# Kernel tuning notes

Hardware: AMD Instinct MI355X
Metric: run time of the kernel (lower is better)

Reference implementation:

```python
import jax, jax.numpy as jnp
import numpy as np

WH, WW = 8, 8          # window_size
NUM_HEADS = 16
DIM = 512
NW = 64                # windows per image (mask leading dim)
BATCH = 16             # images
N = WH * WW            # tokens per window


def _relative_position_index():
    coords = np.stack(np.meshgrid(np.arange(WH), np.arange(WW), indexing='ij'))  # (2,Wh,Ww)
    cf = coords.reshape(2, -1)                                                   # (2,N)
    rel = cf[:, :, None] - cf[:, None, :]                                        # (2,N,N)
    rel = rel.transpose(1, 2, 0).astype(np.int64)                                # (N,N,2)
    rel[:, :, 0] += WH - 1
    rel[:, :, 1] += WW - 1
    rel[:, :, 0] *= 2 * WW - 1
    return jnp.asarray(rel.sum(-1), dtype=jnp.int32)                             # (N,N)


def setup_inputs() -> dict:
    key = jax.random.key(0)
    ks = jax.random.split(key, 8)
    B_ = BATCH * NW
    x = jax.random.normal(ks[0], (B_, N, DIM), dtype=jnp.float32)
    # 0 / -100 additive shift-style mask (Swin uses -100.0 for masked pairs)
    mraw = jax.random.uniform(ks[1], (NW, N, N))
    mask = jnp.where(mraw < 0.15, jnp.float32(-100.0), jnp.float32(0.0))
    qkv_w = jax.random.normal(ks[2], (3 * DIM, DIM), dtype=jnp.float32) * (DIM ** -0.5)
    qkv_b = jnp.zeros((3 * DIM,), dtype=jnp.float32)
    proj_w = jax.random.normal(ks[3], (DIM, DIM), dtype=jnp.float32) * (DIM ** -0.5)
    proj_b = jnp.zeros((DIM,), dtype=jnp.float32)
    n_rel = (2 * WH - 1) * (2 * WW - 1)  # 225
    rpb_table = jax.random.normal(ks[4], (n_rel, NUM_HEADS), dtype=jnp.float32) * 0.02
    rel_index = _relative_position_index()
    return {"x": x, "mask": mask, "qkv_w": qkv_w, "qkv_b": qkv_b,
            "proj_w": proj_w, "proj_b": proj_b, "rpb_table": rpb_table,
            "rel_index": rel_index}


def reference(x, mask, qkv_w, qkv_b, proj_w, proj_b, rpb_table, rel_index):
    B_, n, C = x.shape
    H = NUM_HEADS
    hd = C // H
    scale = hd ** -0.5
    qkv = x @ qkv_w.T + qkv_b                       # (B_, N, 3C)
    qkv = qkv.reshape(B_, n, 3, H, hd)
    q = qkv[:, :, 0].transpose(0, 2, 1, 3) * scale  # (B_, H, N, hd)
    k = qkv[:, :, 1].transpose(0, 2, 1, 3)
    v = qkv[:, :, 2].transpose(0, 2, 1, 3)
    attn = jnp.einsum('bhnd,bhmd->bhnm', q, k)      # (B_, H, N, N)
    bias = rpb_table[rel_index.reshape(-1)].reshape(n, n, H).transpose(2, 0, 1)  # (H,N,N)
    attn = attn + bias[None]
    nW = mask.shape[0]
    attn = attn.reshape(B_ // nW, nW, H, n, n) + mask[None, :, None]
    attn = jax.nn.softmax(attn.reshape(B_, H, n, n), axis=-1)
    out = jnp.einsum('bhnm,bhmd->bhnd', attn, v)    # (B_, H, N, hd)
    out = out.transpose(0, 2, 1, 3).reshape(B_, n, C)
    return out @ proj_w.T + proj_b
```

## Files before the change

### kernel.cpp

```cpp
#include <hip/hip_runtime.h>
#include <hip/hip_bf16.h>

typedef unsigned short u16;
typedef __attribute__((ext_vector_type(8))) short bfrag;
typedef __attribute__((ext_vector_type(4))) float ffrag;

#define NWIN_TOT 1024
#define NTOK 64
#define CDIM 512
#define NHEAD 16
#define HDIM 32
#define NW 64

__device__ __forceinline__ u16 f2bf(float f) {
  union { float f; unsigned u; } v; v.f = f;
  unsigned r = v.u + 0x7fffu + ((v.u >> 16) & 1u);
  return (u16)(r >> 16);
}

__device__ __forceinline__ ffrag mfma16(bfrag a, bfrag b, ffrag c) {
  return __builtin_amdgcn_mfma_f32_16x16x32_bf16(a, b, c, 0, 0, 0);
}

__device__ __forceinline__ void gload16(const u16* src, u16* lds) {
  __builtin_amdgcn_global_load_lds(
      (const __attribute__((address_space(1))) unsigned int*)src,
      (__attribute__((address_space(3))) unsigned int*)lds, 16, 0, 0);
}

#define BAR() __builtin_amdgcn_s_barrier()
#define SCHED0() __builtin_amdgcn_sched_barrier(0)
#define VMW(n) do { asm volatile("s_waitcnt vmcnt(" #n ")" ::: "memory"); \
                    __builtin_amdgcn_sched_barrier(0); } while (0)

__global__ __launch_bounds__(256) void k_prep(const float* __restrict__ x,
                                              const float* __restrict__ qkv_w,
                                              const float* __restrict__ proj_w,
                                              const int*   __restrict__ rel_index,
                                              const float* __restrict__ rpb,
                                              const float* __restrict__ mask,
                                              u16* __restrict__ xb,
                                              u16* __restrict__ wq, u16* __restrict__ wp,
                                              float* __restrict__ biasT,
                                              float* __restrict__ maskT) {
  int i = blockIdx.x * 256 + threadIdx.x;
  if (i < 4194304) {
    int e = i * 8;
    const float4* xp = reinterpret_cast<const float4*>(x + e);
    float4 lo = xp[0], hi = xp[1];
    union { u16 u[8]; bfrag v; } pk;
    pk.u[0] = f2bf(lo.x); pk.u[1] = f2bf(lo.y); pk.u[2] = f2bf(lo.z); pk.u[3] = f2bf(lo.w);
    pk.u[4] = f2bf(hi.x); pk.u[5] = f2bf(hi.y); pk.u[6] = f2bf(hi.z); pk.u[7] = f2bf(hi.w);
    *reinterpret_cast<bfrag*>(xb + e) = pk.v;
    return;
  }
  i -= 4194304;
  if (i < 786432) { wq[i] = f2bf(qkv_w[i]); return; }
  i -= 786432;
  if (i < 262144) { wp[i] = f2bf(proj_w[i]); return; }
  i -= 262144;
  if (i < 65536) {
    int h = i >> 12, rem = i & 4095, c = rem >> 6, r = rem & 63;
    biasT[i] = rpb[rel_index[r * 64 + c] * 16 + h];
    return;
  }
  i -= 65536;
  if (i < 262144) {
    int w0 = i >> 12, c = (i >> 6) & 63, r = i & 63;
    maskT[i] = mask[(w0 << 12) + r * 64 + c];
  }
}

#define MFMAQ(mh, nh, BARR) \
  _Pragma("unroll") for (int i_ = 0; i_ < 4; ++i_) \
  _Pragma("unroll") for (int n_ = 0; n_ < 2; ++n_) \
  _Pragma("unroll") for (int ks_ = 0; ks_ < 2; ++ks_) \
    acc[(mh)*4+i_][(nh)*2+n_] = mfma16(a_[i_*2+ks_], BARR[n_*2+ks_], acc[(mh)*4+i_][(nh)*2+n_]);

template<int EPI>
__global__ __launch_bounds__(512, 2) void k_gemm8(const u16* __restrict__ A,
                                                  const u16* __restrict__ W,
                                                  const float* __restrict__ bias,
                                                  u16* __restrict__ qws, u16* __restrict__ kws,
                                                  u16* __restrict__ vws,
                                                  float* __restrict__ out) {
  constexpr int NT = (EPI == 0) ? 6 : 2;
  constexpr int NWG = 256 * NT;
  extern __shared__ __align__(16) u16 smem[];

  const int bid = blockIdx.x;
  const int tile = (bid & 7) * (NWG >> 3) + (bid >> 3);
  const int bn = tile % NT, bm = tile / NT;
  const int brow = bm << 8, bcol = bn << 8;

  const int tid = threadIdx.x;
  const int wv = tid >> 6, lane = tid & 63, c15 = lane & 15, g = lane >> 4;
  const int wr = wv >> 2, wc = wv & 3;
  const int rowA0 = wr * 128 + c15;
  const int rowB0 = wc * 64 + c15;
  const ffrag zf = {0.f, 0.f, 0.f, 0.f};

  ffrag acc[8][4];
#pragma unroll
  for (int i = 0; i < 8; ++i)
#pragma unroll
    for (int n = 0; n < 4; ++n) acc[i][n] = zf;

  auto stage = [&](int t, int mat, int half) {
    u16* db = smem + ((t & 1) * 2 + mat) * 16384 + half * 8192;
    const u16* gsrc = mat ? W : A;
    const int gr0 = (mat ? bcol : brow) + half * 128;
#pragma unroll
    for (int l = 0; l < 2; ++l) {
      int e = l * 4096 + tid * 8;
      int r = e >> 6, cb = (e & 63) << 1;
      int scol = (cb ^ ((r & 7) << 4)) >> 1;
      gload16(gsrc + (size_t)(gr0 + r) * 512 + t * 64 + scol, db + e);
    }
  };

  stage(0, 0, 0); stage(0, 0, 1); stage(0, 1, 0); stage(0, 1, 1);
  stage(1, 0, 0); stage(1, 0, 1); stage(1, 1, 0); stage(1, 1, 1);
  VMW(8);
  BAR();

  for (int t = 0; t < 8; ++t) {
    const char* As_ = (const char*)(smem + ((t & 1) * 2 + 0) * 16384);
    const char* Bs_ = (const char*)(smem + ((t & 1) * 2 + 1) * 16384);
    bfrag a_[8], b0_[4], b1_[4];

#pragma unroll
    for (int i = 0; i < 4; ++i) {
      int ra = rowA0 + i * 16;
#pragma unroll
      for (int ks = 0; ks < 2; ++ks)
        a_[i * 2 + ks] = *(const bfrag*)(As_ + ra * 128 + ((ks * 64 + g * 16) ^ ((ra & 7) << 4)));
    }
#pragma unroll
    for (int n = 0; n < 2; ++n) {
      int rb = rowB0 + n * 16;
#pragma unroll
      for (int ks = 0; ks < 2; ++ks)
        b0_[n * 2 + ks] = *(const bfrag*)(Bs_ + rb * 128 + ((ks * 64 + g * 16) ^ ((rb & 7) << 4)));
    }
    BAR();
    __builtin_amdgcn_s_setprio(1);
    MFMAQ(0, 0, b0_);
    __builtin_amdgcn_s_setprio(0);
    BAR();

#pragma unroll
    for (int n = 0; n < 2; ++n) {
      int rb = rowB0 + 32 + n * 16;
#pragma unroll
      for (int ks = 0; ks < 2; ++ks)
        b1_[n * 2 + ks] = *(const bfrag*)(Bs_ + rb * 128 + ((ks * 64 + g * 16) ^ ((rb & 7) << 4)));
    }
    BAR();
    __builtin_amdgcn_s_setprio(1);
    MFMAQ(0, 1, b1_);
    __builtin_amdgcn_s_setprio(0);
    BAR();

#pragma unroll
    for (int i = 0; i < 4; ++i) {
      int ra = rowA0 + 64 + i * 16;
#pragma unroll
      for (int ks = 0; ks < 2; ++ks)
        a_[i * 2 + ks] = *(const bfrag*)(As_ + ra * 128 + ((ks * 64 + g * 16) ^ ((ra & 7) << 4)));
    }
    SCHED0();
    if (t + 2 < 8) { stage(t + 2, 1, 0); stage(t + 2, 1, 1); }
    BAR();
    __builtin_amdgcn_s_setprio(1);
    MFMAQ(1, 1, b1_);
    __builtin_amdgcn_s_setprio(0);
    BAR();

    if (t + 2 < 8) { stage(t + 2, 0, 0); stage(t + 2, 0, 1); }
    BAR();
    __builtin_amdgcn_s_setprio(1);
    MFMAQ(1, 0, b0_);
    __builtin_amdgcn_s_setprio(0);
    if (t < 6) { VMW(8); } else if (t == 6) { VMW(0); }
    BAR();
  }

  if (EPI == 0) {
    const float SCALE = 0.17677669529663687f;
    const int win0 = (brow + wr * 128) >> 6;
#pragma unroll
    for (int n = 0; n < 4; ++n) {
      int c = bcol + wc * 64 + n * 16 + c15;
      float bz = bias[c];
      int which = c >> 9;
      int cq = c & 511, h = cq >> 5, d = cq & 31;
      size_t pb0 = ((size_t)(win0 * NHEAD + h)) << 11;
      size_t pb1 = pb0 + ((size_t)NHEAD << 11);
      if (which == 2) {
        u16* v0 = vws + pb0 + (d << 6);
        u16* v1 = vws + pb1 + (d << 6);
#pragma unroll
        for (int i = 0; i < 8; ++i) {
          u16* vp = (i < 4) ? v0 : v1;
#pragma unroll
          for (int r = 0; r < 4; ++r) {
            int tok = (i & 3) * 16 + g * 4 + r;
            vp[tok] = f2bf(acc[i][n][r] + bz);
          }
        }
      } else {
        const float s = (which == 0) ? SCALE : 1.0f;
        u16* base = (which == 0) ? qws : kws;
        u16* q0 = base + pb0 + d;
        u16* q1 = base + pb1 + d;
#pragma unroll
        for (int i = 0; i < 8; ++i) {
          u16* qp = (i < 4) ? q0 : q1;
#pragma unroll
          for (int r = 0; r < 4; ++r) {
            int tok = (i & 3) * 16 + g * 4 + r;
            qp[tok << 5] = f2bf((acc[i][n][r] + bz) * s);
          }
        }
      }
    }
  } else {
#pragma unroll
    for (int n = 0; n < 4; ++n) {
      int c = bcol + wc * 64 + n * 16 + c15;
      float bz = bias[c];
      float* po = out + (size_t)(brow + wr * 128) * CDIM + c;
#pragma unroll
      for (int i = 0; i < 8; ++i)
#pragma unroll
        for (int r = 0; r < 4; ++r)
          po[(size_t)(i * 16 + g * 4 + r) * CDIM] = acc[i][n][r] + bz;
    }
  }
}

__global__ __launch_bounds__(256) void k_attn(const u16* __restrict__ qws,
                                              const u16* __restrict__ kws,
                                              const u16* __restrict__ vws,
                                              const float* __restrict__ biasT,
                                              const float* __restrict__ maskT,
                                              u16* __restrict__ yws) {
  __shared__ __align__(16) u16 plds[4][NTOK * NTOK];
  const int tid = threadIdx.x, w = tid >> 6, lane = tid & 63;
  const int c15 = lane & 15, g = lane >> 4, g4 = g * 4;
  const int p = blockIdx.x * 4 + w;
  const int b = p >> 4, h = p & 15;

  const u16* qb_ = qws + (size_t)p * (NTOK * HDIM);
  const u16* kb_ = kws + (size_t)p * (NTOK * HDIM);
  bfrag qa[4], ka[4];
#pragma unroll
  for (int t = 0; t < 4; ++t) {
    qa[t] = *reinterpret_cast<const bfrag*>(qb_ + (t * 16 + c15) * HDIM + g * 8);
    ka[t] = *reinterpret_cast<const bfrag*>(kb_ + (t * 16 + c15) * HDIM + g * 8);
  }

  const float* bT = biasT + h * 4096;
  const float* mT = maskT + (b & (NW - 1)) * 4096;
  u16* pl = plds[w];
  const ffrag zf = {0.f, 0.f, 0.f, 0.f};

#pragma unroll
  for (int it = 0; it < 4; ++it) {
    int row = it * 16 + c15;
    float l[4][4];
    float mx = -3.0e38f;
#pragma unroll
    for (int jt = 0; jt < 4; ++jt) {
      ffrag s = mfma16(ka[jt], qa[it], zf);
#pragma unroll
      for (int r = 0; r < 4; ++r) {
        int col = jt * 16 + g4 + r;
        float v = s[r] + bT[col * 64 + row] + mT[col * 64 + row];
        l[jt][r] = v;
        mx = fmaxf(mx, v);
      }
    }
    mx = fmaxf(mx, __shfl_xor(mx, 16));
    mx = fmaxf(mx, __shfl_xor(mx, 32));
    float sum = 0.f;
#pragma unroll
    for (int jt = 0; jt < 4; ++jt)
#pragma unroll
      for (int r = 0; r < 4; ++r) {
        float e = __expf(l[jt][r] - mx);
        l[jt][r] = e;
        sum += e;
      }
    sum += __shfl_xor(sum, 16);
    sum += __shfl_xor(sum, 32);
    float inv = 1.0f / sum;
#pragma unroll
    for (int jt = 0; jt < 4; ++jt) {
      union { u16 u[4]; uint2 v; } pk;
#pragma unroll
      for (int r = 0; r < 4; ++r) pk.u[r] = f2bf(l[jt][r] * inv);
      int off = row * 64 + ((jt * 16 + g4) ^ ((row & 7) << 3));
      *reinterpret_cast<uint2*>(&pl[off]) = pk.v;
    }
  }
  __syncthreads();

  const u16* vb_ = vws + (size_t)p * (HDIM * NTOK);
#pragma unroll
  for (int ct = 0; ct < 2; ++ct) {
    ffrag o[4] = {zf, zf, zf, zf};
#pragma unroll
    for (int ks = 0; ks < 2; ++ks) {
      bfrag vf = *reinterpret_cast<const bfrag*>(vb_ + (ct * 16 + c15) * NTOK + ks * 32 + g * 8);
#pragma unroll
      for (int i = 0; i < 4; ++i) {
        int prow = i * 16 + c15;
        bfrag pa = *reinterpret_cast<const bfrag*>(
            &pl[prow * 64 + ((ks * 32 + g * 8) ^ ((prow & 7) << 3))]);
        o[i] = mfma16(pa, vf, o[i]);
      }
    }
#pragma unroll
    for (int i = 0; i < 4; ++i)
#pragma unroll
      for (int r = 0; r < 4; ++r) {
        int tok = i * 16 + g4 + r;
        yws[((size_t)b * NTOK + tok) * CDIM + h * HDIM + ct * 16 + c15] = f2bf(o[i][r]);
      }
  }
}

extern "C" void kernel_launch(void* const* d_in, const int* in_sizes, int n_in,
                              void* d_out, int out_size, void* d_ws, size_t ws_size,
                              hipStream_t stream) {
  const float* x      = (const float*)d_in[0];
  const float* mask   = (const float*)d_in[1];
  const float* qkv_w  = (const float*)d_in[2];
  const float* qkv_b  = (const float*)d_in[3];
  const float* proj_w = (const float*)d_in[4];
  const float* proj_b = (const float*)d_in[5];
  const float* rpb    = (const float*)d_in[6];
  const int*   rel    = (const int*)d_in[7];
  float* out = (float*)d_out;

  char* ws = (char*)d_ws;
  constexpr size_t SZ_QKV = (size_t)NWIN_TOT * NHEAD * NTOK * HDIM * 2;
  u16* qws = (u16*)(ws);
  u16* kws = (u16*)(ws + SZ_QKV);
  u16* vws = (u16*)(ws + 2 * SZ_QKV);
  u16* xb  = (u16*)(ws + 3 * SZ_QKV);
  u16* yws = xb;
  u16* wq  = (u16*)(ws + 4 * SZ_QKV);
  u16* wp  = (u16*)(ws + 4 * SZ_QKV + 1572864);
  float* biasT = (float*)(ws + 4 * SZ_QKV + 1572864 + 524288);
  float* maskT = (float*)(ws + 4 * SZ_QKV + 1572864 + 524288 + 262144);

  hipFuncSetAttribute((const void*)k_gemm8<0>,
                      hipFuncAttributeMaxDynamicSharedMemorySize, 131072);
  hipFuncSetAttribute((const void*)k_gemm8<1>,
                      hipFuncAttributeMaxDynamicSharedMemorySize, 131072);

  k_prep<<<dim3(21760), dim3(256), 0, stream>>>(x, qkv_w, proj_w, rel, rpb, mask,
                                                xb, wq, wp, biasT, maskT);
  k_gemm8<0><<<dim3(256 * 6), dim3(512), 131072, stream>>>(xb, wq, qkv_b, qws, kws, vws, nullptr);
  k_attn<<<dim3(NWIN_TOT * NHEAD / 4), dim3(256), 0, stream>>>(qws, kws, vws, biasT, maskT, yws);
  k_gemm8<1><<<dim3(256 * 2), dim3(512), 131072, stream>>>(yws, wp, proj_b, nullptr, nullptr, nullptr, out);
}
```

Baseline: 351.5 us.

## Precombine bias and mask into bf16 table; prefetch next B fragment in GEMM

The prep kernel now builds a single bf16 table per (window-mask, head) that holds relative-position bias plus the shift mask. The attention kernel then reads one vectorized 8-byte load per tile instead of two scattered fp32 loads per element. The table is larger (64x16x4096 bf16, 8 MB) and bf16 rounding of the bias adds some precision loss. Separately, the GEMM loop loads the first B fragment for the next k-step at the end of the current iteration and moves the vmcnt wait earlier, so shared-memory reads overlap the preceding work.

```diff
diff --git a/kernel.cpp b/kernel.cpp
--- a/kernel.cpp
+++ b/kernel.cpp
@@ -16,6 +16,10 @@
   union { float f; unsigned u; } v; v.f = f;
   unsigned r = v.u + 0x7fffu + ((v.u >> 16) & 1u);
   return (u16)(r >> 16);
+}
+
+__device__ __forceinline__ float bfhi2f(unsigned hi_bits) {
+  union { unsigned u; float f; } v; v.u = hi_bits; return v.f;
 }
 
 __device__ __forceinline__ ffrag mfma16(bfrag a, bfrag b, ffrag c) {
@@ -41,8 +45,7 @@
                                               const float* __restrict__ mask,
                                               u16* __restrict__ xb,
                                               u16* __restrict__ wq, u16* __restrict__ wp,
-                                              float* __restrict__ biasT,
-                                              float* __restrict__ maskT) {
+                                              u16* __restrict__ combB) {
   int i = blockIdx.x * 256 + threadIdx.x;
   if (i < 4194304) {
     int e = i * 8;
@@ -59,15 +62,10 @@
   i -= 786432;
   if (i < 262144) { wp[i] = f2bf(proj_w[i]); return; }
   i -= 262144;
-  if (i < 65536) {
-    int h = i >> 12, rem = i & 4095, c = rem >> 6, r = rem & 63;
-    biasT[i] = rpb[rel_index[r * 64 + c] * 16 + h];
-    return;
-  }
-  i -= 65536;
-  if (i < 262144) {
-    int w0 = i >> 12, c = (i >> 6) & 63, r = i & 63;
-    maskT[i] = mask[(w0 << 12) + r * 64 + c];
+  {
+    int wh = i >> 12, rc = i & 4095;
+    int w0 = wh >> 4, h = wh & 15;
+    combB[i] = f2bf(rpb[rel_index[rc] * 16 + h] + mask[(w0 << 12) + rc]);
   }
 }
 
@@ -124,10 +122,22 @@
   VMW(8);
   BAR();
 
+  bfrag b0_[4];
+  {
+    const char* B0_ = (const char*)(smem + 1 * 16384);
+#pragma unroll
+    for (int n = 0; n < 2; ++n) {
+      int rb = rowB0 + n * 16;
+#pragma unroll
+      for (int ks = 0; ks < 2; ++ks)
+        b0_[n * 2 + ks] = *(const bfrag*)(B0_ + rb * 128 + ((ks * 64 + g * 16) ^ ((rb & 7) << 4)));
+    }
+  }
+
   for (int t = 0; t < 8; ++t) {
     const char* As_ = (const char*)(smem + ((t & 1) * 2 + 0) * 16384);
     const char* Bs_ = (const char*)(smem + ((t & 1) * 2 + 1) * 16384);
-    bfrag a_[8], b0_[4], b1_[4];
+    bfrag a_[8], b1_[4];
 
 #pragma unroll
     for (int i = 0; i < 4; ++i) {
@@ -135,13 +145,6 @@
 #pragma unroll
       for (int ks = 0; ks < 2; ++ks)
         a_[i * 2 + ks] = *(const bfrag*)(As_ + ra * 128 + ((ks * 64 + g * 16) ^ ((ra & 7) << 4)));
-    }
-#pragma unroll
-    for (int n = 0; n < 2; ++n) {
-      int rb = rowB0 + n * 16;
-#pragma unroll
-      for (int ks = 0; ks < 2; ++ks)
-        b0_[n * 2 + ks] = *(const bfrag*)(Bs_ + rb * 128 + ((ks * 64 + g * 16) ^ ((rb & 7) << 4)));
     }
     BAR();
     __builtin_amdgcn_s_setprio(1);
@@ -178,11 +181,21 @@
     BAR();
 
     if (t + 2 < 8) { stage(t + 2, 0, 0); stage(t + 2, 0, 1); }
+    if (t < 6) { VMW(8); } else if (t == 6) { VMW(0); }
     BAR();
     __builtin_amdgcn_s_setprio(1);
     MFMAQ(1, 0, b0_);
     __builtin_amdgcn_s_setprio(0);
-    if (t < 6) { VMW(8); } else if (t == 6) { VMW(0); }
+    if (t < 7) {
+      const char* Bn_ = (const char*)(smem + (((t + 1) & 1) * 2 + 1) * 16384);
+#pragma unroll
+      for (int n = 0; n < 2; ++n) {
+        int rb = rowB0 + n * 16;
+#pragma unroll
+        for (int ks = 0; ks < 2; ++ks)
+          b0_[n * 2 + ks] = *(const bfrag*)(Bn_ + rb * 128 + ((ks * 64 + g * 16) ^ ((rb & 7) << 4)));
+      }
+    }
     BAR();
   }
 
@@ -243,8 +256,7 @@
 __global__ __launch_bounds__(256) void k_attn(const u16* __restrict__ qws,
                                               const u16* __restrict__ kws,
                                               const u16* __restrict__ vws,
-                                              const float* __restrict__ biasT,
-                                              const float* __restrict__ maskT,
+                                              const u16* __restrict__ combB,
                                               u16* __restrict__ yws) {
   __shared__ __align__(16) u16 plds[4][NTOK * NTOK];
   const int tid = threadIdx.x, w = tid >> 6, lane = tid & 63;
@@ -261,8 +273,7 @@
     ka[t] = *reinterpret_cast<const bfrag*>(kb_ + (t * 16 + c15) * HDIM + g * 8);
   }
 
-  const float* bT = biasT + h * 4096;
-  const float* mT = maskT + (b & (NW - 1)) * 4096;
+  const u16* cB = combB + ((size_t)(((b & (NW - 1)) << 4) + h) << 12);
   u16* pl = plds[w];
   const ffrag zf = {0.f, 0.f, 0.f, 0.f};
 
@@ -274,13 +285,16 @@
 #pragma unroll
     for (int jt = 0; jt < 4; ++jt) {
       ffrag s = mfma16(ka[jt], qa[it], zf);
-#pragma unroll
-      for (int r = 0; r < 4; ++r) {
-        int col = jt * 16 + g4 + r;
-        float v = s[r] + bT[col * 64 + row] + mT[col * 64 + row];
-        l[jt][r] = v;
-        mx = fmaxf(mx, v);
-      }
+      uint2 cw = *reinterpret_cast<const uint2*>(cB + row * 64 + jt * 16 + g4);
+      float c0 = bfhi2f(cw.x << 16);
+      float c1 = bfhi2f(cw.x & 0xffff0000u);
+      float c2 = bfhi2f(cw.y << 16);
+      float c3 = bfhi2f(cw.y & 0xffff0000u);
+      l[jt][0] = s[0] + c0;
+      l[jt][1] = s[1] + c1;
+      l[jt][2] = s[2] + c2;
+      l[jt][3] = s[3] + c3;
+      mx = fmaxf(mx, fmaxf(fmaxf(l[jt][0], l[jt][1]), fmaxf(l[jt][2], l[jt][3])));
     }
     mx = fmaxf(mx, __shfl_xor(mx, 16));
     mx = fmaxf(mx, __shfl_xor(mx, 32));
@@ -354,17 +368,16 @@
   u16* yws = xb;
   u16* wq  = (u16*)(ws + 4 * SZ_QKV);
   u16* wp  = (u16*)(ws + 4 * SZ_QKV + 1572864);
-  float* biasT = (float*)(ws + 4 * SZ_QKV + 1572864 + 524288);
-  float* maskT = (float*)(ws + 4 * SZ_QKV + 1572864 + 524288 + 262144);
+  u16* combB = (u16*)(ws + 4 * SZ_QKV + 1572864 + 524288);
 
   hipFuncSetAttribute((const void*)k_gemm8<0>,
                       hipFuncAttributeMaxDynamicSharedMemorySize, 131072);
   hipFuncSetAttribute((const void*)k_gemm8<1>,
                       hipFuncAttributeMaxDynamicSharedMemorySize, 131072);
 
-  k_prep<<<dim3(21760), dim3(256), 0, stream>>>(x, qkv_w, proj_w, rel, rpb, mask,
-                                                xb, wq, wp, biasT, maskT);
+  k_prep<<<dim3(36864), dim3(256), 0, stream>>>(x, qkv_w, proj_w, rel, rpb, mask,
+                                                xb, wq, wp, combB);
   k_gemm8<0><<<dim3(256 * 6), dim3(512), 131072, stream>>>(xb, wq, qkv_b, qws, kws, vws, nullptr);
-  k_attn<<<dim3(NWIN_TOT * NHEAD / 4), dim3(256), 0, stream>>>(qws, kws, vws, biasT, maskT, yws);
+  k_attn<<<dim3(NWIN_TOT * NHEAD / 4), dim3(256), 0, stream>>>(qws, kws, vws, combB, yws);
   k_gemm8<1><<<dim3(256 * 2), dim3(512), 131072, stream>>>(yws, wp, proj_b, nullptr, nullptr, nullptr, out);
 }
```

Result: faster. 310.3 us (-11.7%).
